# Kernel optimization log

Hardware: AMD Instinct MI355X
Metric: run time of the kernel (lower is better)

## Reference

```python
import jax, jax.numpy as jnp
import numpy as np

B, N, K, C_IN, OC = 16, 4096, 16, 64, 64
OC2 = OC // 2
LEAK = 0.2
EPS = 1e-12  # guards sqrt grad when a neighbor equals the center point


def _cbn(x, w, s, b):
    # 1x1 conv (channel-last) + folded eval-mode BatchNorm: (x @ w.T) * s + b
    return jnp.einsum('...i,oi->...o', x, w) * s + b


def _lrelu(x):
    return jax.nn.leaky_relu(x, LEAK)


def _gather(feat, idx):
    # feat [B,N,C], idx [B,N,k] -> [B,N,k,C]  (index_points)
    return jax.vmap(lambda f, i: f[i])(feat, idx)


def _attentive_pool(x_info, feat, idx, wq, sq, bq, wk, sk, bk, wv, sv, bv, w2, s2, b2):
    q = jax.nn.relu(_cbn(feat, wq, sq, bq))   # [B,N,C]
    kf = jax.nn.relu(_cbn(feat, wk, sk, bk))
    vf = jax.nn.relu(_cbn(feat, wv, sv, bv))
    Kn = _gather(kf, idx)                     # [B,N,k,C]
    W = x_info * (Kn - q[:, :, None, :])      # [B,N,k,C]
    Vn = _gather(vf, idx)
    a = jax.nn.softmax(W, axis=2)             # softmax over k neighbors
    out = jnp.sum(a * Vn, axis=2)             # [B,N,C]
    return _lrelu(_cbn(out, w2, s2, b2))


def _forward(x, feature, neighbor_index,
             mlp1_w, mlp1_s, mlp1_b, lse1_w, lse1_s, lse1_b,
             p1_wq, p1_sq, p1_bq, p1_wk, p1_sk, p1_bk, p1_wv, p1_sv, p1_bv, p1_w2, p1_s2, p1_b2,
             lse2_w, lse2_s, lse2_b,
             p2_wq, p2_sq, p2_bq, p2_wk, p2_sk, p2_bk, p2_wv, p2_sv, p2_bv, p2_w2, p2_s2, p2_b2,
             mlp2_w, mlp2_s, mlp2_b, res_w, res_s, res_b):
    idx = neighbor_index
    xt = jnp.transpose(x, (0, 2, 1))          # [B,N,3]
    ft = jnp.transpose(feature, (0, 2, 1))    # [B,N,C_IN]
    identity = ft
    f1 = _lrelu(_cbn(ft, mlp1_w, mlp1_s, mlp1_b))        # [B,N,OC2]
    knn_x = _gather(xt, idx)                             # [B,N,k,3]
    center = jnp.broadcast_to(xt[:, :, None, :], knn_x.shape)
    diff = knn_x - center
    dist = jnp.sqrt(jnp.sum(diff * diff, axis=-1, keepdims=True) + EPS)  # [B,N,k,1]
    x_info = jnp.concatenate([center, knn_x, diff, dist], axis=-1)       # [B,N,k,10]
    x_info = _lrelu(_cbn(x_info, lse1_w, lse1_s, lse1_b))                # [B,N,k,OC2]
    feat2 = _attentive_pool(x_info, f1, idx,
                            p1_wq, p1_sq, p1_bq, p1_wk, p1_sk, p1_bk,
                            p1_wv, p1_sv, p1_bv, p1_w2, p1_s2, p1_b2)    # [B,N,OC2]
    x_info2 = _lrelu(_cbn(x_info, lse2_w, lse2_s, lse2_b))               # [B,N,k,OC2]
    feat3 = _attentive_pool(x_info2, feat2, idx,
                            p2_wq, p2_sq, p2_bq, p2_wk, p2_sk, p2_bk,
                            p2_wv, p2_sv, p2_bv, p2_w2, p2_s2, p2_b2)    # [B,N,OC]
    out = _cbn(feat3, mlp2_w, mlp2_s, mlp2_b)            # [B,N,2*OC]
    res = _cbn(identity, res_w, res_s, res_b)            # [B,N,2*OC]
    out = _lrelu(out + res)
    return jnp.transpose(out, (0, 2, 1))                 # [B,2*OC,N]


def setup_inputs() -> dict:
    key = jax.random.key(0)
    it = iter(jax.random.split(key, 80))
    nxt = lambda: next(it)

    def w(*shape):
        return jax.random.normal(nxt(), shape, jnp.float32) * 0.1

    def bn(c):
        s = jax.random.uniform(nxt(), (c,), jnp.float32, 0.5, 1.5)
        b = jax.random.normal(nxt(), (c,), jnp.float32) * 0.1
        return s, b

    inp = {
        'x': jax.random.normal(nxt(), (B, 3, N), jnp.float32),
        'feature': jax.random.normal(nxt(), (B, C_IN, N), jnp.float32),
        'neighbor_index': jax.random.randint(nxt(), (B, N, K), 0, N, jnp.int32),
    }
    inp['mlp1_w'] = w(OC2, C_IN); inp['mlp1_s'], inp['mlp1_b'] = bn(OC2)
    inp['lse1_w'] = w(OC2, 10); inp['lse1_s'], inp['lse1_b'] = bn(OC2)
    for p, co in (('p1', OC2), ('p2', OC)):
        inp[p + '_wq'] = w(OC2, OC2); inp[p + '_sq'], inp[p + '_bq'] = bn(OC2)
        inp[p + '_wk'] = w(OC2, OC2); inp[p + '_sk'], inp[p + '_bk'] = bn(OC2)
        inp[p + '_wv'] = w(OC2, OC2); inp[p + '_sv'], inp[p + '_bv'] = bn(OC2)
        inp[p + '_w2'] = w(co, OC2); inp[p + '_s2'], inp[p + '_b2'] = bn(co)
    inp['lse2_w'] = w(OC2, OC2); inp['lse2_s'], inp['lse2_b'] = bn(OC2)
    inp['mlp2_w'] = w(2 * OC, OC); inp['mlp2_s'], inp['mlp2_b'] = bn(2 * OC)
    inp['res_w'] = w(2 * OC, C_IN); inp['res_s'], inp['res_b'] = bn(2 * OC)
    return inp


def reference(x, feature, neighbor_index,
              mlp1_w, mlp1_s, mlp1_b, lse1_w, lse1_s, lse1_b,
              p1_wq, p1_sq, p1_bq, p1_wk, p1_sk, p1_bk, p1_wv, p1_sv, p1_bv, p1_w2, p1_s2, p1_b2,
              lse2_w, lse2_s, lse2_b,
              p2_wq, p2_sq, p2_bq, p2_wk, p2_sk, p2_bk, p2_wv, p2_sv, p2_bv, p2_w2, p2_s2, p2_b2,
              mlp2_w, mlp2_s, mlp2_b, res_w, res_s, res_b):
    return _forward(x, feature, neighbor_index,
                    mlp1_w, mlp1_s, mlp1_b, lse1_w, lse1_s, lse1_b,
                    p1_wq, p1_sq, p1_bq, p1_wk, p1_sk, p1_bk, p1_wv, p1_sv, p1_bv, p1_w2, p1_s2, p1_b2,
                    lse2_w, lse2_s, lse2_b,
                    p2_wq, p2_sq, p2_bq, p2_wk, p2_sk, p2_bk, p2_wv, p2_sv, p2_bv, p2_w2, p2_s2, p2_b2,
                    mlp2_w, mlp2_s, mlp2_b, res_w, res_s, res_b)
```

## Files before the change

### kernel.cpp

```cpp
#include <hip/hip_runtime.h>
#include <cstdint>
#include <cstddef>

#define NB 16
#define NP 4096
#define KNN 16
#define CIN 64
#define H 32
#define OCC 64
#define PN ((size_t)NB*NP)

__device__ __forceinline__ float lrelu(float v){ return v > 0.f ? v : 0.2f*v; }
__device__ __forceinline__ float reluf(float v){ return v > 0.f ? v : 0.f; }

typedef __attribute__((ext_vector_type(8)))  short bf16x8s;
typedef __attribute__((ext_vector_type(4)))  float f32x4;
typedef __attribute__((ext_vector_type(16))) float f32x16;

__device__ __forceinline__ short f2bf(float f){
    union { float f; unsigned u; } v; v.f = f;
    unsigned r = v.u + 0x7fffu + ((v.u >> 16) & 1u);
    return (short)(r >> 16);
}

__device__ __forceinline__ bf16x8s pack8(float4 a, float4 b, float sc){
    bf16x8s r;
    r[0]=f2bf(a.x*sc); r[1]=f2bf(a.y*sc); r[2]=f2bf(a.z*sc); r[3]=f2bf(a.w*sc);
    r[4]=f2bf(b.x*sc); r[5]=f2bf(b.y*sc); r[6]=f2bf(b.z*sc); r[7]=f2bf(b.w*sc);
    return r;
}

__global__ __launch_bounds__(256) void k_pointwise(
    const float* __restrict__ feat, const float* __restrict__ xpos,
    const float* __restrict__ w1, const float* __restrict__ s1, const float* __restrict__ b1,
    const float* __restrict__ wq, const float* __restrict__ sq, const float* __restrict__ bq,
    const float* __restrict__ wk, const float* __restrict__ sk, const float* __restrict__ bk,
    const float* __restrict__ wv, const float* __restrict__ sv, const float* __restrict__ bv,
    float* __restrict__ q1, float* __restrict__ kv1,
    float* __restrict__ xp, short* __restrict__ ftp)
{
    __shared__ float ftile[CIN][65];
    __shared__ float f1t[H][65];
    int t = threadIdx.x;
    int l = t & 63;
    int g = __builtin_amdgcn_readfirstlane(t >> 6);
    int bid = blockIdx.x;
    int b  = bid >> 6;
    int n0 = (bid & 63) * 64;
    int n  = n0 + l;
    size_t p = (size_t)b*NP + n;

    const float* fb = feat + ((size_t)b*CIN)*NP + n;
    float fv[16];
    #pragma unroll
    for (int k=0;k<16;k++){
        int c = g*16 + k;
        fv[k] = fb[(size_t)c*NP];
        ftile[c][l] = fv[k];
    }
    {
        bf16x8s h0, h1;
        #pragma unroll
        for (int i=0;i<8;i++){ h0[i] = f2bf(fv[i]); h1[i] = f2bf(fv[8+i]); }
        *(bf16x8s*)(ftp + p*64 + g*16)     = h0;
        *(bf16x8s*)(ftp + p*64 + g*16 + 8) = h1;
    }
    if (g == 0){
        const float* xb = xpos + (size_t)b*3*NP;
        *(float4*)(xp + 4*p) = make_float4(xb[n], xb[NP+n], xb[2*NP+n], 0.f);
    }
    __syncthreads();

    float acc[8];
    #pragma unroll
    for (int u=0;u<8;u++) acc[u] = 0.f;
    #pragma unroll
    for (int c=0;c<CIN;c++){
        float x = ftile[c][l];
        #pragma unroll
        for (int u=0;u<8;u++) acc[u] = fmaf(w1[(g*8+u)*CIN+c], x, acc[u]);
    }
    #pragma unroll
    for (int u=0;u<8;u++){
        int h = g*8+u;
        f1t[h][l] = lrelu(acc[u]*s1[h] + b1[h]);
    }
    __syncthreads();

    float aq[8], ak[8], av[8];
    #pragma unroll
    for (int u=0;u<8;u++){ aq[u]=0.f; ak[u]=0.f; av[u]=0.f; }
    #pragma unroll
    for (int j=0;j<H;j++){
        float x = f1t[j][l];
        #pragma unroll
        for (int u=0;u<8;u++){
            int h = g*8+u;
            aq[u] = fmaf(wq[h*H+j], x, aq[u]);
            ak[u] = fmaf(wk[h*H+j], x, ak[u]);
            av[u] = fmaf(wv[h*H+j], x, av[u]);
        }
    }
    float qr[8], kr[8], vr[8];
    #pragma unroll
    for (int u=0;u<8;u++){
        int h = g*8+u;
        qr[u] = reluf(aq[u]*sq[h]+bq[h]);
        kr[u] = reluf(ak[u]*sk[h]+bk[h]);
        vr[u] = reluf(av[u]*sv[h]+bv[h]);
    }
    size_t qb = p*H + g*8;
    *(float4*)(q1+qb)   = make_float4(qr[0],qr[1],qr[2],qr[3]);
    *(float4*)(q1+qb+4) = make_float4(qr[4],qr[5],qr[6],qr[7]);
    size_t kb = (p*H + g*8)*2;
    #pragma unroll
    for (int u2=0;u2<4;u2++)
        *(float4*)(kv1+kb+u2*4) = make_float4(kr[u2*2],vr[u2*2],kr[u2*2+1],vr[u2*2+1]);
}

__global__ __launch_bounds__(256) void k_pool1(
    const float* __restrict__ xp, const int* __restrict__ nidx,
    const float* __restrict__ q1, const float* __restrict__ kv1,
    const float* __restrict__ l1w, const float* __restrict__ l1s, const float* __restrict__ l1b,
    const float* __restrict__ w2, const float* __restrict__ s2, const float* __restrict__ b2,
    const float* __restrict__ wq, const float* __restrict__ sq, const float* __restrict__ bq,
    const float* __restrict__ wk, const float* __restrict__ sk, const float* __restrict__ bk,
    const float* __restrict__ wv, const float* __restrict__ sv, const float* __restrict__ bv,
    float* __restrict__ q2, float* __restrict__ kv2)
{
    __shared__ float wl[4][32*36];
    __shared__ float bcp[4][2][32];
    __shared__ float bcf[4][2][32];
    int t = threadIdx.x;
    {
        const float* wsrc[4] = {w2, wq, wk, wv};
        #pragma unroll
        for (int m=0;m<4;m++)
            for (int i=t;i<1024;i+=256)
                wl[m][(i>>5)*36 + (i&31)] = wsrc[m][i];
    }
    __syncthreads();

    int wv_ = t >> 6;
    int l   = t & 63;
    int n_  = l & 31;
    int hi  = l >> 5;
    int bid = blockIdx.x;
    int sb  = ((bid & 7) << 10) | (bid >> 3);
    size_t p0 = (size_t)sb*8 + (size_t)wv_*2;
    int b = (int)(p0 >> 12);

    bf16x8s Bf;
    if (hi == 0){
        #pragma unroll
        for (int i=0;i<8;i++) Bf[i] = f2bf(l1w[n_*10 + i]);
    } else {
        Bf[0] = f2bf(l1w[n_*10 + 8]);
        Bf[1] = f2bf(l1w[n_*10 + 9]);
        #pragma unroll
        for (int i=2;i<8;i++) Bf[i] = 0;
    }

    int ptA  = (l >> 4) & 1;
    int nbrA = l & 15;
    size_t pA = p0 + ptA;
    int idA = nidx[pA*KNN + nbrA];
    float4 cp = *(const float4*)(xp + 4*pA);
    float4 nv = *(const float4*)(xp + 4*((size_t)(b<<12)+idA));
    float dx = nv.x-cp.x, dy = nv.y-cp.y, dz = nv.z-cp.z;
    float dist = sqrtf(dx*dx+dy*dy+dz*dz + 1e-12f);
    bf16x8s A;
    if (hi == 0){
        A[0]=f2bf(cp.x); A[1]=f2bf(cp.y); A[2]=f2bf(cp.z); A[3]=f2bf(nv.x);
        A[4]=f2bf(nv.y); A[5]=f2bf(nv.z); A[6]=f2bf(dx);   A[7]=f2bf(dy);
    } else {
        A[0]=f2bf(dz); A[1]=f2bf(dist);
        A[2]=0; A[3]=0; A[4]=0; A[5]=0; A[6]=0; A[7]=0;
    }

    f32x16 cz = {0.f,0.f,0.f,0.f,0.f,0.f,0.f,0.f,0.f,0.f,0.f,0.f,0.f,0.f,0.f,0.f};
    f32x16 D = __builtin_amdgcn_mfma_f32_32x32x16_bf16(A, Bf, cz, 0, 0, 0);

    float sl1 = l1s[n_], bl1 = l1b[n_];
    const int* irow0 = nidx + p0*KNN;
    float outv[2];
    #pragma unroll
    for (int pt=0; pt<2; pt++){
        size_t p = p0 + pt;
        float qc = q1[p*H + n_];
        int4 idlo = *(const int4*)(irow0 + pt*KNN + 4*hi);
        int4 idhi = *(const int4*)(irow0 + pt*KNN + 8 + 4*hi);
        int ids[8] = {idlo.x,idlo.y,idlo.z,idlo.w, idhi.x,idhi.y,idhi.z,idhi.w};
        float W[8], V[8];
        #pragma unroll
        for (int rr=0; rr<8; rr++){
            float xi = lrelu(D[pt*8+rr]*sl1 + bl1);
            float2 kv = *(const float2*)(kv1 + 2*(((size_t)b*NP + ids[rr])*H + n_));
            W[rr] = xi*(kv.x - qc);
            V[rr] = kv.y;
        }
        float mx = W[0];
        #pragma unroll
        for (int rr=1;rr<8;rr++) mx = fmaxf(mx, W[rr]);
        mx = fmaxf(mx, __shfl_xor(mx, 32, 64));
        float den = 0.f, ac = 0.f;
        #pragma unroll
        for (int rr=0;rr<8;rr++){
            float e = __expf(W[rr]-mx);
            den += e; ac = fmaf(e, V[rr], ac);
        }
        den += __shfl_xor(den, 32, 64);
        ac  += __shfl_xor(ac,  32, 64);
        outv[pt] = ac/den;
    }
    if (l < 32){ bcp[wv_][0][n_] = outv[0]; bcp[wv_][1][n_] = outv[1]; }

    int c = n_;
    float f2a = 0.f;
    #pragma unroll
    for (int jj=0;jj<8;jj++){
        float4 xv = *(const float4*)&bcp[wv_][hi][jj*4];
        float4 w4 = *(const float4*)&wl[0][c*36 + jj*4];
        f2a += w4.x*xv.x + w4.y*xv.y + w4.z*xv.z + w4.w*xv.w;
    }
    float f2 = lrelu(f2a*s2[c] + b2[c]);
    bcf[wv_][hi][c] = f2;

    float aq=0.f, ak=0.f, av=0.f;
    #pragma unroll
    for (int jj=0;jj<8;jj++){
        float4 xv  = *(const float4*)&bcf[wv_][hi][jj*4];
        float4 wq4 = *(const float4*)&wl[1][c*36 + jj*4];
        float4 wk4 = *(const float4*)&wl[2][c*36 + jj*4];
        float4 wv4 = *(const float4*)&wl[3][c*36 + jj*4];
        aq += wq4.x*xv.x + wq4.y*xv.y + wq4.z*xv.z + wq4.w*xv.w;
        ak += wk4.x*xv.x + wk4.y*xv.y + wk4.z*xv.z + wk4.w*xv.w;
        av += wv4.x*xv.x + wv4.y*xv.y + wv4.z*xv.z + wv4.w*xv.w;
    }
    size_t base = (p0 + hi)*H + c;
    q2[base] = reluf(aq*sq[c]+bq[c]);
    *(float2*)(kv2 + 2*base) = make_float2(reluf(ak*sk[c]+bk[c]), reluf(av*sv[c]+bv[c]));
}

__global__ __launch_bounds__(256) void k_pool2(
    const float* __restrict__ xp, const int* __restrict__ nidx,
    const float* __restrict__ q2, const float* __restrict__ kv2,
    const float* __restrict__ l1w, const float* __restrict__ l1s, const float* __restrict__ l1b,
    const float* __restrict__ l2w, const float* __restrict__ l2s, const float* __restrict__ l2b,
    const float* __restrict__ w2, const float* __restrict__ s2, const float* __restrict__ b2,
    short* __restrict__ f3)
{
    __shared__ float we[64*36];
    __shared__ float bc[4][2][32];
    __shared__ unsigned short xiT[4][32*40];
    int t = threadIdx.x;
    for (int i=t;i<2048;i+=256) we[(i>>5)*36 + (i&31)] = w2[i];
    __syncthreads();

    int wv_ = t >> 6;
    int l   = t & 63;
    int n_  = l & 31;
    int hi  = l >> 5;
    int bid = blockIdx.x;
    int sb  = ((bid & 7) << 10) | (bid >> 3);
    size_t p0 = (size_t)sb*8 + (size_t)wv_*2;
    int b = (int)(p0 >> 12);

    bf16x8s Bf1;
    if (hi == 0){
        #pragma unroll
        for (int i=0;i<8;i++) Bf1[i] = f2bf(l1w[n_*10 + i]);
    } else {
        Bf1[0] = f2bf(l1w[n_*10 + 8]);
        Bf1[1] = f2bf(l1w[n_*10 + 9]);
        #pragma unroll
        for (int i=2;i<8;i++) Bf1[i] = 0;
    }
    int ptA  = (l >> 4) & 1;
    int nbrA = l & 15;
    size_t pA = p0 + ptA;
    int idA = nidx[pA*KNN + nbrA];
    float4 cp = *(const float4*)(xp + 4*pA);
    float4 nv = *(const float4*)(xp + 4*((size_t)(b<<12)+idA));
    float dx = nv.x-cp.x, dy = nv.y-cp.y, dz = nv.z-cp.z;
    float dist = sqrtf(dx*dx+dy*dy+dz*dz + 1e-12f);
    bf16x8s Ag;
    if (hi == 0){
        Ag[0]=f2bf(cp.x); Ag[1]=f2bf(cp.y); Ag[2]=f2bf(cp.z); Ag[3]=f2bf(nv.x);
        Ag[4]=f2bf(nv.y); Ag[5]=f2bf(nv.z); Ag[6]=f2bf(dx);   Ag[7]=f2bf(dy);
    } else {
        Ag[0]=f2bf(dz); Ag[1]=f2bf(dist);
        Ag[2]=0; Ag[3]=0; Ag[4]=0; Ag[5]=0; Ag[6]=0; Ag[7]=0;
    }
    f32x16 cz = {0.f,0.f,0.f,0.f,0.f,0.f,0.f,0.f,0.f,0.f,0.f,0.f,0.f,0.f,0.f,0.f};
    f32x16 D1 = __builtin_amdgcn_mfma_f32_32x32x16_bf16(Ag, Bf1, cz, 0, 0, 0);

    float sl1 = l1s[n_], bl1 = l1b[n_];
    #pragma unroll
    for (int r=0;r<16;r++){
        int m = (r&3) + 8*(r>>2) + 4*hi;
        xiT[wv_][m*40 + n_] = (unsigned short)f2bf(lrelu(D1[r]*sl1 + bl1));
    }
    bf16x8s A20 = *(const bf16x8s*)&xiT[wv_][n_*40 + hi*8];
    bf16x8s A21 = *(const bf16x8s*)&xiT[wv_][n_*40 + 16 + hi*8];

    bf16x8s B0, B1;
    {
        const float* r0 = l2w + n_*32 + hi*8;
        #pragma unroll
        for (int i=0;i<8;i++){ B0[i] = f2bf(r0[i]); B1[i] = f2bf(r0[16+i]); }
    }
    f32x16 D = __builtin_amdgcn_mfma_f32_32x32x16_bf16(A20, B0, cz, 0, 0, 0);
    D = __builtin_amdgcn_mfma_f32_32x32x16_bf16(A21, B1, D, 0, 0, 0);

    float sl2 = l2s[n_], bl2 = l2b[n_];
    const int* irow0 = nidx + p0*KNN;
    float outv[2];
    #pragma unroll
    for (int pt=0; pt<2; pt++){
        size_t p = p0 + pt;
        float qc = q2[p*H + n_];
        int4 idlo = *(const int4*)(irow0 + pt*KNN + 4*hi);
        int4 idhi = *(const int4*)(irow0 + pt*KNN + 8 + 4*hi);
        int ids[8] = {idlo.x,idlo.y,idlo.z,idlo.w, idhi.x,idhi.y,idhi.z,idhi.w};
        float W[8], V[8];
        #pragma unroll
        for (int rr=0; rr<8; rr++){
            float xi2 = lrelu(D[pt*8+rr]*sl2 + bl2);
            float2 kv = *(const float2*)(kv2 + 2*(((size_t)b*NP + ids[rr])*H + n_));
            W[rr] = xi2*(kv.x - qc);
            V[rr] = kv.y;
        }
        float mx = W[0];
        #pragma unroll
        for (int rr=1;rr<8;rr++) mx = fmaxf(mx, W[rr]);
        mx = fmaxf(mx, __shfl_xor(mx, 32, 64));
        float den = 0.f, ac = 0.f;
        #pragma unroll
        for (int rr=0;rr<8;rr++){
            float e = __expf(W[rr]-mx);
            den += e; ac = fmaf(e, V[rr], ac);
        }
        den += __shfl_xor(den, 32, 64);
        ac  += __shfl_xor(ac,  32, 64);
        outv[pt] = ac/den;
    }
    if (l < 32){ bc[wv_][0][n_] = outv[0]; bc[wv_][1][n_] = outv[1]; }

    float fa=0.f, fb2=0.f;
    #pragma unroll
    for (int jj=0;jj<8;jj++){
        float4 xv  = *(const float4*)&bc[wv_][hi][jj*4];
        float4 wa4 = *(const float4*)&we[n_*36 + jj*4];
        float4 wb4 = *(const float4*)&we[(n_+32)*36 + jj*4];
        fa  += wa4.x*xv.x + wa4.y*xv.y + wa4.z*xv.z + wa4.w*xv.w;
        fb2 += wb4.x*xv.x + wb4.y*xv.y + wb4.z*xv.z + wb4.w*xv.w;
    }
    size_t pp = p0 + hi;
    f3[pp*64 + n_]      = f2bf(lrelu(fa *s2[n_]    + b2[n_]));
    f3[pp*64 + 32 + n_] = f2bf(lrelu(fb2*s2[n_+32] + b2[n_+32]));
}

__global__ __launch_bounds__(256) void k_final(
    const short* __restrict__ ftp, const short* __restrict__ f3,
    const float* __restrict__ m2w, const float* __restrict__ m2s, const float* __restrict__ m2b,
    const float* __restrict__ rw, const float* __restrict__ rs, const float* __restrict__ rb,
    float* __restrict__ out)
{
    int t = threadIdx.x;
    int l  = t & 63;
    int w  = t >> 6;
    int lr = l & 15;
    int lg = l >> 4;
    int ot0 = w * 32;

    bf16x8s A[2][4];
    float bias[2][4];
    #pragma unroll
    for (int mt=0; mt<2; mt++){
        int o = ot0 + mt*16 + lr;
        float scm = m2s[o], scr = rs[o];
        const float* pm = m2w + (size_t)o*64 + lg*8;
        const float* pr = rw  + (size_t)o*64 + lg*8;
        #pragma unroll
        for (int kk=0;kk<2;kk++)
            A[mt][kk] = pack8(*(const float4*)(pm + kk*32),
                              *(const float4*)(pm + kk*32 + 4), scm);
        #pragma unroll
        for (int kk=0;kk<2;kk++)
            A[mt][2+kk] = pack8(*(const float4*)(pr + kk*32),
                                *(const float4*)(pr + kk*32 + 4), scr);
        int od = ot0 + mt*16 + lg*4;
        #pragma unroll
        for (int r=0;r<4;r++) bias[mt][r] = m2b[od+r] + rb[od+r];
    }

    size_t pbase = (size_t)blockIdx.x * 64;
    int b = (int)(pbase >> 12);
    float* ob = out + ((size_t)b*128)*NP;

    #pragma unroll
    for (int ti=0; ti<4; ti++){
        size_t p0 = pbase + ti*16;
        int n0 = (int)(p0 & (NP-1));
        const short* fp3 = f3  + (p0 + lr)*64 + lg*8;
        const short* fpt = ftp + (p0 + lr)*64 + lg*8;
        bf16x8s Bf[4];
        Bf[0] = *(const bf16x8s*)(fp3);
        Bf[1] = *(const bf16x8s*)(fp3 + 32);
        Bf[2] = *(const bf16x8s*)(fpt);
        Bf[3] = *(const bf16x8s*)(fpt + 32);
        #pragma unroll
        for (int mt=0;mt<2;mt++){
            f32x4 D = {0.f,0.f,0.f,0.f};
            #pragma unroll
            for (int kk=0;kk<4;kk++)
                D = __builtin_amdgcn_mfma_f32_16x16x32_bf16(A[mt][kk], Bf[kk], D, 0, 0, 0);
            #pragma unroll
            for (int r=0;r<4;r++){
                int od = ot0 + mt*16 + lg*4 + r;
                ob[(size_t)od*NP + n0 + lr] = lrelu(D[r] + bias[mt][r]);
            }
        }
    }
}

extern "C" void kernel_launch(void* const* d_in, const int* in_sizes, int n_in,
                              void* d_out, int out_size, void* d_ws, size_t ws_size,
                              hipStream_t stream)
{
    (void)in_sizes; (void)n_in; (void)out_size; (void)ws_size;
    const float* x     = (const float*)d_in[0];
    const float* feat  = (const float*)d_in[1];
    const int*   nidx  = (const int*)  d_in[2];
    const float* m1w=(const float*)d_in[3],  *m1s=(const float*)d_in[4],  *m1b=(const float*)d_in[5];
    const float* l1w=(const float*)d_in[6],  *l1s=(const float*)d_in[7],  *l1b=(const float*)d_in[8];
    const float* p1wq=(const float*)d_in[9],  *p1sq=(const float*)d_in[10], *p1bq=(const float*)d_in[11];
    const float* p1wk=(const float*)d_in[12], *p1sk=(const float*)d_in[13], *p1bk=(const float*)d_in[14];
    const float* p1wv=(const float*)d_in[15], *p1sv=(const float*)d_in[16], *p1bv=(const float*)d_in[17];
    const float* p1w2=(const float*)d_in[18], *p1s2=(const float*)d_in[19], *p1b2=(const float*)d_in[20];
    const float* p2wq=(const float*)d_in[21], *p2sq=(const float*)d_in[22], *p2bq=(const float*)d_in[23];
    const float* p2wk=(const float*)d_in[24], *p2sk=(const float*)d_in[25], *p2bk=(const float*)d_in[26];
    const float* p2wv=(const float*)d_in[27], *p2sv=(const float*)d_in[28], *p2bv=(const float*)d_in[29];
    const float* p2w2=(const float*)d_in[30], *p2s2=(const float*)d_in[31], *p2b2=(const float*)d_in[32];
    const float* l2w=(const float*)d_in[33], *l2s=(const float*)d_in[34], *l2b=(const float*)d_in[35];
    const float* m2w=(const float*)d_in[36], *m2s=(const float*)d_in[37], *m2b=(const float*)d_in[38];
    const float* rw =(const float*)d_in[39], *rs =(const float*)d_in[40], *rb =(const float*)d_in[41];

    float* ws = (float*)d_ws;
    float* q1  = ws;
    float* kv1 = ws + PN*32;
    float* q2  = ws + PN*96;
    float* kv2 = ws + PN*128;
    float* xp  = ws + PN*192;
    short* ftp = (short*)(ws + PN*196);
    short* f3  = (short*)ws;

    float* outp = (float*)d_out;

    k_pointwise<<<dim3(PN/64),dim3(256),0,stream>>>(feat, x, m1w,m1s,m1b,
        p1wq,p1sq,p1bq, p1wk,p1sk,p1bk, p1wv,p1sv,p1bv, q1,kv1, xp, ftp);
    k_pool1<<<dim3(PN/8),dim3(256),0,stream>>>(xp,nidx, q1,kv1,
        l1w,l1s,l1b, p1w2,p1s2,p1b2,
        p2wq,p2sq,p2bq, p2wk,p2sk,p2bk, p2wv,p2sv,p2bv, q2,kv2);
    k_pool2<<<dim3(PN/8),dim3(256),0,stream>>>(xp,nidx, q2,kv2,
        l1w,l1s,l1b, l2w,l2s,l2b, p2w2,p2s2,p2b2, f3);
    k_final<<<dim3(PN/64),dim3(256),0,stream>>>(ftp, f3, m2w,m2s,m2b, rw,rs,rb, outp);
}
```

Baseline: 303.2 us.

## Fuse final MLP and residual projection into second pooling kernel

Merges k_final into k_pool2 so that each 512-thread block handles 16 points. The pool-2 output goes through its w2 conv with an MFMA into shared memory, followed by the combined mlp2 and residual 1x1 convs via MFMA, and the result is written straight to the output. The mlp2/residual weights and the p2_w2 weights are pre-converted to bf16, and the biases are summed once, by block 0 of the pointwise kernel. This removes the f3 intermediate round-trip and one kernel launch. The cost is extra block-level syncs and lower parallelism in the epilogue, where only 4 of 8 waves run the w2 MFMA. The 16-point tiles also write only 16 contiguous floats per output row.

```diff
diff --git a/kernel.cpp b/kernel.cpp
--- a/kernel.cpp
+++ b/kernel.cpp
@@ -23,13 +23,6 @@
     return (short)(r >> 16);
 }
 
-__device__ __forceinline__ bf16x8s pack8(float4 a, float4 b, float sc){
-    bf16x8s r;
-    r[0]=f2bf(a.x*sc); r[1]=f2bf(a.y*sc); r[2]=f2bf(a.z*sc); r[3]=f2bf(a.w*sc);
-    r[4]=f2bf(b.x*sc); r[5]=f2bf(b.y*sc); r[6]=f2bf(b.z*sc); r[7]=f2bf(b.w*sc);
-    return r;
-}
-
 __global__ __launch_bounds__(256) void k_pointwise(
     const float* __restrict__ feat, const float* __restrict__ xpos,
     const float* __restrict__ w1, const float* __restrict__ s1, const float* __restrict__ b1,
@@ -37,7 +30,11 @@
     const float* __restrict__ wk, const float* __restrict__ sk, const float* __restrict__ bk,
     const float* __restrict__ wv, const float* __restrict__ sv, const float* __restrict__ bv,
     float* __restrict__ q1, float* __restrict__ kv1,
-    float* __restrict__ xp, short* __restrict__ ftp)
+    float* __restrict__ xp, short* __restrict__ ftp,
+    const float* __restrict__ m2w, const float* __restrict__ m2s, const float* __restrict__ m2b,
+    const float* __restrict__ rw, const float* __restrict__ rs, const float* __restrict__ rb,
+    const float* __restrict__ p2w2,
+    short* __restrict__ wbigW, short* __restrict__ w2bW, float* __restrict__ bbW)
 {
     __shared__ float ftile[CIN][65];
     __shared__ float f1t[H][65];
@@ -116,6 +113,28 @@
     #pragma unroll
     for (int u2=0;u2<4;u2++)
         *(float4*)(kv1+kb+u2*4) = make_float4(kr[u2*2],vr[u2*2],kr[u2*2+1],vr[u2*2+1]);
+
+    if (bid == 0){
+        int o = t >> 1, half = t & 1;
+        const float* srcp = half ? (rw + (size_t)o*64) : (m2w + (size_t)o*64);
+        float sc = half ? rs[o] : m2s[o];
+        short* dst = wbigW + (size_t)o*128 + half*64;
+        #pragma unroll
+        for (int j=0;j<64;j+=8){
+            bf16x8s v8;
+            #pragma unroll
+            for (int i=0;i<8;i++) v8[i] = f2bf(srcp[j+i]*sc);
+            *(bf16x8s*)(dst + j) = v8;
+        }
+        if (!half) bbW[o] = m2b[o] + rb[o];
+        {
+            int i0 = t*8;
+            bf16x8s w8;
+            #pragma unroll
+            for (int i=0;i<8;i++) w8[i] = f2bf(p2w2[i0+i]);
+            *(bf16x8s*)(w2bW + i0) = w8;
+        }
+    }
 }
 
 __global__ __launch_bounds__(256) void k_pool1(
@@ -242,29 +261,28 @@
     *(float2*)(kv2 + 2*base) = make_float2(reluf(ak*sk[c]+bk[c]), reluf(av*sv[c]+bv[c]));
 }
 
-__global__ __launch_bounds__(256) void k_pool2(
+__global__ __launch_bounds__(512) void k_pool2(
     const float* __restrict__ xp, const int* __restrict__ nidx,
     const float* __restrict__ q2, const float* __restrict__ kv2,
     const float* __restrict__ l1w, const float* __restrict__ l1s, const float* __restrict__ l1b,
     const float* __restrict__ l2w, const float* __restrict__ l2s, const float* __restrict__ l2b,
-    const float* __restrict__ w2, const float* __restrict__ s2, const float* __restrict__ b2,
-    short* __restrict__ f3)
+    const short* __restrict__ w2bf, const float* __restrict__ s2, const float* __restrict__ b2,
+    const short* __restrict__ ftp, const short* __restrict__ wbig, const float* __restrict__ bb,
+    float* __restrict__ out)
 {
-    __shared__ float we[64*36];
-    __shared__ float bc[4][2][32];
-    __shared__ unsigned short xiT[4][32*40];
+    __shared__ unsigned short xiT[8][32*40];
+    __shared__ unsigned short bcb[16][40];
+    __shared__ unsigned short xf[16][72];
     int t = threadIdx.x;
-    for (int i=t;i<2048;i+=256) we[(i>>5)*36 + (i&31)] = w2[i];
-    __syncthreads();
-
     int wv_ = t >> 6;
     int l   = t & 63;
     int n_  = l & 31;
     int hi  = l >> 5;
     int bid = blockIdx.x;
-    int sb  = ((bid & 7) << 10) | (bid >> 3);
-    size_t p0 = (size_t)sb*8 + (size_t)wv_*2;
-    int b = (int)(p0 >> 12);
+    int sb  = ((bid & 7) << 9) | (bid >> 3);
+    size_t pbase = (size_t)sb * 16;
+    size_t p0 = pbase + (size_t)wv_*2;
+    int b = (int)(pbase >> 12);
 
     bf16x8s Bf1;
     if (hi == 0){
@@ -303,7 +321,6 @@
     }
     bf16x8s A20 = *(const bf16x8s*)&xiT[wv_][n_*40 + hi*8];
     bf16x8s A21 = *(const bf16x8s*)&xiT[wv_][n_*40 + 16 + hi*8];
-
     bf16x8s B0, B1;
     {
         const float* r0 = l2w + n_*32 + hi*8;
@@ -345,84 +362,51 @@
         ac  += __shfl_xor(ac,  32, 64);
         outv[pt] = ac/den;
     }
-    if (l < 32){ bc[wv_][0][n_] = outv[0]; bc[wv_][1][n_] = outv[1]; }
-
-    float fa=0.f, fb2=0.f;
-    #pragma unroll
-    for (int jj=0;jj<8;jj++){
-        float4 xv  = *(const float4*)&bc[wv_][hi][jj*4];
-        float4 wa4 = *(const float4*)&we[n_*36 + jj*4];
-        float4 wb4 = *(const float4*)&we[(n_+32)*36 + jj*4];
-        fa  += wa4.x*xv.x + wa4.y*xv.y + wa4.z*xv.z + wa4.w*xv.w;
-        fb2 += wb4.x*xv.x + wb4.y*xv.y + wb4.z*xv.z + wb4.w*xv.w;
-    }
-    size_t pp = p0 + hi;
-    f3[pp*64 + n_]      = f2bf(lrelu(fa *s2[n_]    + b2[n_]));
-    f3[pp*64 + 32 + n_] = f2bf(lrelu(fb2*s2[n_+32] + b2[n_+32]));
-}
-
-__global__ __launch_bounds__(256) void k_final(
-    const short* __restrict__ ftp, const short* __restrict__ f3,
-    const float* __restrict__ m2w, const float* __restrict__ m2s, const float* __restrict__ m2b,
-    const float* __restrict__ rw, const float* __restrict__ rs, const float* __restrict__ rb,
-    float* __restrict__ out)
-{
-    int t = threadIdx.x;
-    int l  = t & 63;
-    int w  = t >> 6;
-    int lr = l & 15;
-    int lg = l >> 4;
-    int ot0 = w * 32;
-
-    bf16x8s A[2][4];
-    float bias[2][4];
-    #pragma unroll
-    for (int mt=0; mt<2; mt++){
-        int o = ot0 + mt*16 + lr;
-        float scm = m2s[o], scr = rs[o];
-        const float* pm = m2w + (size_t)o*64 + lg*8;
-        const float* pr = rw  + (size_t)o*64 + lg*8;
-        #pragma unroll
-        for (int kk=0;kk<2;kk++)
-            A[mt][kk] = pack8(*(const float4*)(pm + kk*32),
-                              *(const float4*)(pm + kk*32 + 4), scm);
-        #pragma unroll
-        for (int kk=0;kk<2;kk++)
-            A[mt][2+kk] = pack8(*(const float4*)(pr + kk*32),
-                                *(const float4*)(pr + kk*32 + 4), scr);
-        int od = ot0 + mt*16 + lg*4;
-        #pragma unroll
-        for (int r=0;r<4;r++) bias[mt][r] = m2b[od+r] + rb[od+r];
-    }
-
-    size_t pbase = (size_t)blockIdx.x * 64;
-    int b = (int)(pbase >> 12);
-    float* ob = out + ((size_t)b*128)*NP;
-
-    #pragma unroll
-    for (int ti=0; ti<4; ti++){
-        size_t p0 = pbase + ti*16;
-        int n0 = (int)(p0 & (NP-1));
-        const short* fp3 = f3  + (p0 + lr)*64 + lg*8;
-        const short* fpt = ftp + (p0 + lr)*64 + lg*8;
-        bf16x8s Bf[4];
-        Bf[0] = *(const bf16x8s*)(fp3);
-        Bf[1] = *(const bf16x8s*)(fp3 + 32);
-        Bf[2] = *(const bf16x8s*)(fpt);
-        Bf[3] = *(const bf16x8s*)(fpt + 32);
-        #pragma unroll
-        for (int mt=0;mt<2;mt++){
-            f32x4 D = {0.f,0.f,0.f,0.f};
-            #pragma unroll
-            for (int kk=0;kk<4;kk++)
-                D = __builtin_amdgcn_mfma_f32_16x16x32_bf16(A[mt][kk], Bf[kk], D, 0, 0, 0);
-            #pragma unroll
-            for (int r=0;r<4;r++){
-                int od = ot0 + mt*16 + lg*4 + r;
-                ob[(size_t)od*NP + n0 + lr] = lrelu(D[r] + bias[mt][r]);
-            }
-        }
-    }
+    if (l < 32){
+        bcb[wv_*2 + 0][n_] = (unsigned short)f2bf(outv[0]);
+        bcb[wv_*2 + 1][n_] = (unsigned short)f2bf(outv[1]);
+    }
+    __syncthreads();
+
+    int lr = l & 15, kg = l >> 4;
+    if (wv_ < 4){
+        bf16x8s Aw = *(const bf16x8s*)(w2bf + (wv_*16 + lr)*32 + kg*8);
+        bf16x8s Bp = *(const bf16x8s*)&bcb[lr][kg*8];
+        f32x4 zz = {0.f,0.f,0.f,0.f};
+        f32x4 Df = __builtin_amdgcn_mfma_f32_16x16x32_bf16(Aw, Bp, zz, 0, 0, 0);
+        int ch0 = wv_*16 + kg*4;
+        float4 s4 = *(const float4*)(s2 + ch0);
+        float4 b4 = *(const float4*)(b2 + ch0);
+        xf[lr][ch0+0] = (unsigned short)f2bf(lrelu(Df[0]*s4.x + b4.x));
+        xf[lr][ch0+1] = (unsigned short)f2bf(lrelu(Df[1]*s4.y + b4.y));
+        xf[lr][ch0+2] = (unsigned short)f2bf(lrelu(Df[2]*s4.z + b4.z));
+        xf[lr][ch0+3] = (unsigned short)f2bf(lrelu(Df[3]*s4.w + b4.w));
+    }
+    __syncthreads();
+
+    int o0 = wv_ * 16;
+    const short* wr = wbig + (size_t)(o0 + lr)*128 + kg*8;
+    bf16x8s Af0 = *(const bf16x8s*)(wr);
+    bf16x8s Af1 = *(const bf16x8s*)(wr + 32);
+    bf16x8s Af2 = *(const bf16x8s*)(wr + 64);
+    bf16x8s Af3 = *(const bf16x8s*)(wr + 96);
+    bf16x8s Bx0 = *(const bf16x8s*)&xf[lr][kg*8];
+    bf16x8s Bx1 = *(const bf16x8s*)&xf[lr][32 + kg*8];
+    const short* fr = ftp + (pbase + lr)*64 + kg*8;
+    bf16x8s Bx2 = *(const bf16x8s*)(fr);
+    bf16x8s Bx3 = *(const bf16x8s*)(fr + 32);
+    f32x4 Dq = {0.f,0.f,0.f,0.f};
+    Dq = __builtin_amdgcn_mfma_f32_16x16x32_bf16(Af0, Bx0, Dq, 0, 0, 0);
+    Dq = __builtin_amdgcn_mfma_f32_16x16x32_bf16(Af1, Bx1, Dq, 0, 0, 0);
+    Dq = __builtin_amdgcn_mfma_f32_16x16x32_bf16(Af2, Bx2, Dq, 0, 0, 0);
+    Dq = __builtin_amdgcn_mfma_f32_16x16x32_bf16(Af3, Bx3, Dq, 0, 0, 0);
+    float4 bb4 = *(const float4*)(bb + o0 + kg*4);
+    int n0 = (int)(pbase & (NP-1));
+    float* ob = out + ((size_t)b*128)*NP + n0 + lr;
+    ob[(size_t)(o0 + kg*4 + 0)*NP] = lrelu(Dq[0] + bb4.x);
+    ob[(size_t)(o0 + kg*4 + 1)*NP] = lrelu(Dq[1] + bb4.y);
+    ob[(size_t)(o0 + kg*4 + 2)*NP] = lrelu(Dq[2] + bb4.z);
+    ob[(size_t)(o0 + kg*4 + 3)*NP] = lrelu(Dq[3] + bb4.w);
 }
 
 extern "C" void kernel_launch(void* const* d_in, const int* in_sizes, int n_in,
@@ -454,16 +438,18 @@
     float* kv2 = ws + PN*128;
     float* xp  = ws + PN*192;
     short* ftp = (short*)(ws + PN*196);
-    short* f3  = (short*)ws;
+    short* wbig = (short*)(ws + PN*228);
+    short* w2bf = wbig + 16384;
+    float* bb   = (float*)(w2bf + 2048);
 
     float* outp = (float*)d_out;
 
     k_pointwise<<<dim3(PN/64),dim3(256),0,stream>>>(feat, x, m1w,m1s,m1b,
-        p1wq,p1sq,p1bq, p1wk,p1sk,p1bk, p1wv,p1sv,p1bv, q1,kv1, xp, ftp);
+        p1wq,p1sq,p1bq, p1wk,p1sk,p1bk, p1wv,p1sv,p1bv, q1,kv1, xp, ftp,
+        m2w,m2s,m2b, rw,rs,rb, p2w2, wbig, w2bf, bb);
     k_pool1<<<dim3(PN/8),dim3(256),0,stream>>>(xp,nidx, q1,kv1,
         l1w,l1s,l1b, p1w2,p1s2,p1b2,
         p2wq,p2sq,p2bq, p2wk,p2sk,p2bk, p2wv,p2sv,p2bv, q2,kv2);
-    k_pool2<<<dim3(PN/8),dim3(256),0,stream>>>(xp,nidx, q2,kv2,
-        l1w,l1s,l1b, l2w,l2s,l2b, p2w2,p2s2,p2b2, f3);
-    k_final<<<dim3(PN/64),dim3(256),0,stream>>>(ftp, f3, m2w,m2s,m2b, rw,rs,rb, outp);
+    k_pool2<<<dim3(PN/16),dim3(512),0,stream>>>(xp,nidx, q2,kv2,
+        l1w,l1s,l1b, l2w,l2s,l2b, w2bf, p2s2, p2b2, ftp, wbig, bb, outp);
 }
```

Measured after the change: 301.9 us. About the same (-0.4%).
